# Kernel optimization log

Measured on AMD Instinct MI355X. Metric: run time of the kernel, lower is better.

## Reference

```python
import jax, jax.numpy as jnp
import numpy as np

N = 100000      # nodes
E = 1_000_000   # edges (avg degree ~10)
D_IN = 64
HID = 64
N_CLS = 32


def setup_inputs() -> dict:
    key = jax.random.key(0)
    ks = jax.random.split(key, 9)
    x = jax.random.normal(ks[0], (N, D_IN), dtype=jnp.float32)
    edge_index = jax.random.randint(ks[1], (2, E), 0, N, dtype=jnp.int32)
    s_in = 1.0 / np.sqrt(D_IN)
    s_h = 1.0 / np.sqrt(HID)
    W1 = jax.random.normal(ks[2], (D_IN, HID), dtype=jnp.float32) * s_in
    b1 = jnp.zeros((HID,), dtype=jnp.float32)
    W2 = jax.random.normal(ks[3], (HID, HID), dtype=jnp.float32) * s_h
    b2 = jnp.zeros((HID,), dtype=jnp.float32)
    Wl = jax.random.normal(ks[4], (HID, N_CLS), dtype=jnp.float32) * s_h
    bl = jnp.zeros((N_CLS,), dtype=jnp.float32)
    return {"x": x, "edge_index": edge_index,
            "W1": W1, "b1": b1, "W2": W2, "b2": b2, "Wl": Wl, "bl": bl}


def reference(x, edge_index, W1, b1, W2, b2, Wl, bl):
    # GCNConv default: add self-loops, symmetric normalization D^-1/2 (A+I) D^-1/2
    loop = jnp.arange(N, dtype=edge_index.dtype)
    src = jnp.concatenate([edge_index[0], loop])  # [E+N]
    dst = jnp.concatenate([edge_index[1], loop])  # [E+N]

    deg = jax.ops.segment_sum(jnp.ones_like(dst, dtype=jnp.float32), dst,
                              num_segments=N)              # [N]
    dinv = jnp.where(deg > 0, jax.lax.rsqrt(deg), 0.0)      # D^-1/2
    norm = dinv[src] * dinv[dst]                            # [E+N]

    def gcn_conv(h, W, b):
        h = h @ W                                           # [N, F_out]
        msg = h[src] * norm[:, None]                        # gather + scale
        return jax.ops.segment_sum(msg, dst, num_segments=N) + b

    h = jax.nn.relu(gcn_conv(x, W1, b1))
    h = jax.nn.relu(gcn_conv(h, W2, b2))
    return h @ Wl + bl
```

## Files before the change

### kernel.cpp

```cpp
#include <hip/hip_runtime.h>
#include <hip/hip_fp16.h>
#include <math.h>


#define TPB    256
#define EBLKS  256
#define BSH    9
#define BNODES (1 << BSH)

__global__ __launch_bounds__(TPB)
void k_p1hist(const int* __restrict__ dst, int* __restrict__ OFS,
              int E, int CH, int NBC) {
    __shared__ int h[512];
    int tid = threadIdx.x, b = blockIdx.x;
    for (int i = tid; i < NBC; i += TPB) h[i] = 0;
    __syncthreads();
    int beg = b * CH, end = min(E, beg + CH);
    if (beg < end) {
        int nfull = (end - beg) & ~3;
        for (int i = beg + tid * 4; i < beg + nfull; i += TPB * 4) {
            int4 d = *(const int4*)&dst[i];
            atomicAdd(&h[d.x >> BSH], 1);
            atomicAdd(&h[d.y >> BSH], 1);
            atomicAdd(&h[d.z >> BSH], 1);
            atomicAdd(&h[d.w >> BSH], 1);
        }
        if (tid < (end - beg) - nfull)
            atomicAdd(&h[dst[beg + nfull + tid] >> BSH], 1);
    }
    __syncthreads();
    for (int c = tid; c < NBC; c += TPB) OFS[c * EBLKS + b] = h[c];
}

__global__ __launch_bounds__(TPB)
void k_scanA(const int* __restrict__ OFS, int* __restrict__ bsum, int total) {
    __shared__ int s[TPB];
    int tid = threadIdx.x;
    int i0  = blockIdx.x * 1024 + tid * 4;
    int t = 0;
#pragma unroll
    for (int k = 0; k < 4; ++k) {
        int i = i0 + k;
        t += (i < total) ? OFS[i] : 0;
    }
    s[tid] = t;
    __syncthreads();
    for (int off = TPB / 2; off > 0; off >>= 1) {
        if (tid < off) s[tid] += s[tid + off];
        __syncthreads();
    }
    if (tid == 0) bsum[blockIdx.x] = s[0];
}

__global__ __launch_bounds__(TPB)
void k_scanB(int* bsum, int* OFS, int NBLK, int total, int E) {
    __shared__ int s[TPB];
    int tid = threadIdx.x;
    int v = (tid < NBLK) ? bsum[tid] : 0;
    s[tid] = v;
    __syncthreads();
    for (int off = 1; off < TPB; off <<= 1) {
        int x = (tid >= off) ? s[tid - off] : 0;
        __syncthreads();
        s[tid] += x;
        __syncthreads();
    }
    if (tid < NBLK) bsum[tid] = s[tid] - v;
    if (tid == 0) OFS[total] = E;
}

__global__ __launch_bounds__(TPB)
void k_scanC(int* __restrict__ OFS, const int* __restrict__ bsum, int total) {
    __shared__ int s[TPB];
    int tid = threadIdx.x;
    int i0  = blockIdx.x * 1024 + tid * 4;
    int v[4];
#pragma unroll
    for (int k = 0; k < 4; ++k) {
        int i = i0 + k;
        v[k] = (i < total) ? OFS[i] : 0;
    }
    int tsum = v[0] + v[1] + v[2] + v[3];
    s[tid] = tsum;
    __syncthreads();
    for (int off = 1; off < TPB; off <<= 1) {
        int x = (tid >= off) ? s[tid - off] : 0;
        __syncthreads();
        s[tid] += x;
        __syncthreads();
    }
    int base = bsum[blockIdx.x] + (s[tid] - tsum);
#pragma unroll
    for (int k = 0; k < 4; ++k) {
        int i = i0 + k;
        if (i < total) {
            OFS[i] = base;
            base += v[k];
        }
    }
}

__global__ __launch_bounds__(TPB)
void k_p1scatter(const int* __restrict__ src, const int* __restrict__ dst,
                 const int* __restrict__ OFS, int* __restrict__ ebuf,
                 int E, int CH, int NBC) {
    __shared__ int cur[512];
    int tid = threadIdx.x, b = blockIdx.x;
    for (int c = tid; c < NBC; c += TPB) cur[c] = OFS[c * EBLKS + b];
    __syncthreads();
    int beg = b * CH, end = min(E, beg + CH);
    if (beg >= end) return;
    int nfull = (end - beg) & ~3;
    for (int i = beg + tid * 4; i < beg + nfull; i += TPB * 4) {
        int4 s4 = *(const int4*)&src[i];
        int4 d4 = *(const int4*)&dst[i];
        int p0 = atomicAdd(&cur[d4.x >> BSH], 1);
        int p1 = atomicAdd(&cur[d4.y >> BSH], 1);
        int p2 = atomicAdd(&cur[d4.z >> BSH], 1);
        int p3 = atomicAdd(&cur[d4.w >> BSH], 1);
        ebuf[p0] = (s4.x << BSH) | (d4.x & (BNODES - 1));
        ebuf[p1] = (s4.y << BSH) | (d4.y & (BNODES - 1));
        ebuf[p2] = (s4.z << BSH) | (d4.z & (BNODES - 1));
        ebuf[p3] = (s4.w << BSH) | (d4.w & (BNODES - 1));
    }
    if (tid < (end - beg) - nfull) {
        int i = beg + nfull + tid;
        int d = dst[i];
        int p = atomicAdd(&cur[d >> BSH], 1);
        ebuf[p] = (src[i] << BSH) | (d & (BNODES - 1));
    }
}

__global__ __launch_bounds__(TPB)
void k_p2rowptr(const int* __restrict__ ebuf, const int* __restrict__ OFS,
                int* __restrict__ row_ptr, float* __restrict__ dinv,
                int N, int E, int NBC) {
    __shared__ int cnt[BNODES];
    __shared__ int s1[TPB];
    int tid = threadIdx.x, c = blockIdx.x;
    int beg = OFS[c * EBLKS], end = OFS[(c + 1) * EBLKS];
    for (int i = tid; i < BNODES; i += TPB) cnt[i] = 0;
    __syncthreads();
    for (int i = beg + tid; i < end; i += TPB)
        atomicAdd(&cnt[ebuf[i] & (BNODES - 1)], 1);
    __syncthreads();
    int a0 = cnt[2 * tid], a1 = cnt[2 * tid + 1];
    int pairsum = a0 + a1;
    s1[tid] = pairsum;
    __syncthreads();
    for (int off = 1; off < TPB; off <<= 1) {
        int x = (tid >= off) ? s1[tid - off] : 0;
        __syncthreads();
        s1[tid] += x;
        __syncthreads();
    }
    int ex = s1[tid] - pairsum;
    int node0 = (c << BSH) + 2 * tid;
    if (node0 < N) {
        row_ptr[node0] = beg + ex;
        dinv[node0]    = rsqrtf((float)(a0 + 1));
    }
    if (node0 + 1 < N) {
        row_ptr[node0 + 1] = beg + ex + a0;
        dinv[node0 + 1]    = rsqrtf((float)(a1 + 1));
    }
    if (c == NBC - 1 && tid == 0) row_ptr[N] = E;
}

__global__ __launch_bounds__(TPB)
void k_p2fill(const int* __restrict__ ebuf, const int* __restrict__ OFS,
              const int* __restrict__ row_ptr, const float* __restrict__ dinv,
              int2* __restrict__ colw, int NBC) {
    __shared__ int cnt[BNODES];
    int tid = threadIdx.x, c = blockIdx.x;
    int beg = OFS[c * EBLKS], end = OFS[(c + 1) * EBLKS];
    int cbase = c << BSH;
    for (int i = tid; i < BNODES; i += TPB) cnt[i] = 0;
    __syncthreads();
    for (int i0 = beg + tid; i0 < end; i0 += TPB * 4) {
        int   sv[4], dl[4], pos[4];
        float w[4];
        int   have = 0;
#pragma unroll
        for (int k = 0; k < 4; ++k) {
            int i = i0 + k * TPB;
            if (i < end) {
                int e = ebuf[i];
                sv[k] = e >> BSH;
                dl[k] = e & (BNODES - 1);
                have = k + 1;
            }
        }
#pragma unroll
        for (int k = 0; k < 4; ++k) {
            if (k < have) {
                int r  = atomicAdd(&cnt[dl[k]], 1);
                pos[k] = row_ptr[cbase + dl[k]] + r;
                w[k]   = dinv[sv[k]] * dinv[cbase + dl[k]];
            }
        }
#pragma unroll
        for (int k = 0; k < 4; ++k)
            if (k < have) colw[pos[k]] = make_int2(sv[k], __float_as_int(w[k]));
    }
}

template <int F, bool FINAL, bool HIN, bool HOUT>
__launch_bounds__(256)
__global__ void k_mm(const void* __restrict__ in, const float* __restrict__ W,
                     const float* __restrict__ bias,
                     void* __restrict__ t_out, int n) {
    __shared__ float in_s[64 * 68];
    __shared__ float w_s[64 * F];

    const int tid  = threadIdx.x;
    const int row0 = blockIdx.x * 64;

    for (int i4 = tid; i4 < (64 * F) / 4; i4 += 256)
        ((float4*)w_s)[i4] = ((const float4*)W)[i4];

    if constexpr (HIN) {
        for (int idx = tid; idx < 64 * 8; idx += 256) {
            int r  = idx >> 3;
            int c8 = idx & 7;
            uint4 u = make_uint4(0u, 0u, 0u, 0u);
            if (row0 + r < n)
                u = *(const uint4*)((const __half*)in + (size_t)(row0 + r) * 64 + c8 * 8);
            float2 f0 = __half22float2(*(__half2*)&u.x);
            float2 f1 = __half22float2(*(__half2*)&u.y);
            float2 f2 = __half22float2(*(__half2*)&u.z);
            float2 f3 = __half22float2(*(__half2*)&u.w);
            float* o = &in_s[r * 68 + c8 * 8];
            *(float4*)&o[0] = make_float4(f0.x, f0.y, f1.x, f1.y);
            *(float4*)&o[4] = make_float4(f2.x, f2.y, f3.x, f3.y);
        }
    } else {
        for (int idx = tid; idx < 64 * 16; idx += 256) {
            int r  = idx >> 4;
            int c4 = idx & 15;
            float4 v;
            if (row0 + r < n)
                v = *(const float4*)((const float*)in + (size_t)(row0 + r) * 64 + c4 * 4);
            else
                v = make_float4(0.f, 0.f, 0.f, 0.f);
            *(float4*)&in_s[r * 68 + c4 * 4] = v;
        }
    }
    __syncthreads();

    constexpr int CPT = F / 16;
    const int tx = tid & 15;
    const int ty = tid >> 4;

    float acc[4][CPT];
#pragma unroll
    for (int r = 0; r < 4; ++r)
#pragma unroll
        for (int c = 0; c < CPT; ++c) acc[r][c] = 0.f;

#pragma unroll 4
    for (int k = 0; k < 64; ++k) {
        float b[CPT];
#pragma unroll
        for (int c = 0; c < CPT; ++c) b[c] = w_s[k * F + tx * CPT + c];
#pragma unroll
        for (int r = 0; r < 4; ++r) {
            float a = in_s[(ty * 4 + r) * 68 + k];
#pragma unroll
            for (int c = 0; c < CPT; ++c) acc[r][c] = fmaf(a, b[c], acc[r][c]);
        }
    }

#pragma unroll
    for (int r = 0; r < 4; ++r) {
        int row = row0 + ty * 4 + r;
        if (row >= n) continue;
        if constexpr (HOUT) {
            __half2 p0 = __floats2half2_rn(acc[r][0], acc[r][1]);
            __half2 p1 = __floats2half2_rn(acc[r][2], acc[r][3]);
            uint2 u = make_uint2(*(unsigned*)&p0, *(unsigned*)&p1);
            *(uint2*)((__half*)t_out + (size_t)row * 64 + tx * 4) = u;
        } else {
#pragma unroll
            for (int c = 0; c < CPT; ++c) {
                int col = tx * CPT + c;
                float v = acc[r][c];
                if constexpr (FINAL) v += bias[col];
                ((float*)t_out)[(size_t)row * F + col] = v;
            }
        }
    }
}

__global__ __launch_bounds__(256)
void k_gather(const int* __restrict__ row_ptr, const int2* __restrict__ colw,
              const float* __restrict__ dinv, const float* __restrict__ bias,
              const __half* __restrict__ t, __half* __restrict__ agg, int N) {
    int tid  = threadIdx.x;
    int w    = tid >> 6;
    int lane = tid & 63;
    int g = lane >> 3;
    int p = lane & 7;
    int d = blockIdx.x * 32 + w * 8 + g;

    int beg = 0, end = 0;
    if (d < N) { beg = row_ptr[d]; end = row_ptr[d + 1]; }

    float acc[8];
#pragma unroll
    for (int k = 0; k < 8; ++k) acc[k] = 0.f;

    for (int e = beg; e < end; e += 2) {
        int2 cw0 = colw[e];
        int2 cw1 = (e + 1 < end) ? colw[e + 1] : make_int2(0, 0);
        uint4 a0 = *(const uint4*)(t + (size_t)cw0.x * 64 + p * 8);
        uint4 a1 = *(const uint4*)(t + (size_t)cw1.x * 64 + p * 8);
        float w0 = __int_as_float(cw0.y);
        float w1 = __int_as_float(cw1.y);
        float2 f;
        f = __half22float2(*(__half2*)&a0.x); acc[0] = fmaf(w0, f.x, acc[0]); acc[1] = fmaf(w0, f.y, acc[1]);
        f = __half22float2(*(__half2*)&a0.y); acc[2] = fmaf(w0, f.x, acc[2]); acc[3] = fmaf(w0, f.y, acc[3]);
        f = __half22float2(*(__half2*)&a0.z); acc[4] = fmaf(w0, f.x, acc[4]); acc[5] = fmaf(w0, f.y, acc[5]);
        f = __half22float2(*(__half2*)&a0.w); acc[6] = fmaf(w0, f.x, acc[6]); acc[7] = fmaf(w0, f.y, acc[7]);
        f = __half22float2(*(__half2*)&a1.x); acc[0] = fmaf(w1, f.x, acc[0]); acc[1] = fmaf(w1, f.y, acc[1]);
        f = __half22float2(*(__half2*)&a1.y); acc[2] = fmaf(w1, f.x, acc[2]); acc[3] = fmaf(w1, f.y, acc[3]);
        f = __half22float2(*(__half2*)&a1.z); acc[4] = fmaf(w1, f.x, acc[4]); acc[5] = fmaf(w1, f.y, acc[5]);
        f = __half22float2(*(__half2*)&a1.w); acc[6] = fmaf(w1, f.x, acc[6]); acc[7] = fmaf(w1, f.y, acc[7]);
    }

    if (d < N) {
        float dd = dinv[d];
        float w2 = dd * dd;
        uint4 a = *(const uint4*)(t + (size_t)d * 64 + p * 8);
        float4 b0 = *(const float4*)&bias[p * 8];
        float4 b1 = *(const float4*)&bias[p * 8 + 4];
        float2 s0 = __half22float2(*(__half2*)&a.x);
        float2 s1 = __half22float2(*(__half2*)&a.y);
        float2 s2 = __half22float2(*(__half2*)&a.z);
        float2 s3 = __half22float2(*(__half2*)&a.w);
        float o0 = fmaxf(fmaf(w2, s0.x, acc[0]) + b0.x, 0.f);
        float o1 = fmaxf(fmaf(w2, s0.y, acc[1]) + b0.y, 0.f);
        float o2 = fmaxf(fmaf(w2, s1.x, acc[2]) + b0.z, 0.f);
        float o3 = fmaxf(fmaf(w2, s1.y, acc[3]) + b0.w, 0.f);
        float o4 = fmaxf(fmaf(w2, s2.x, acc[4]) + b1.x, 0.f);
        float o5 = fmaxf(fmaf(w2, s2.y, acc[5]) + b1.y, 0.f);
        float o6 = fmaxf(fmaf(w2, s3.x, acc[6]) + b1.z, 0.f);
        float o7 = fmaxf(fmaf(w2, s3.y, acc[7]) + b1.w, 0.f);
        __half2 h0 = __floats2half2_rn(o0, o1);
        __half2 h1 = __floats2half2_rn(o2, o3);
        __half2 h2 = __floats2half2_rn(o4, o5);
        __half2 h3 = __floats2half2_rn(o6, o7);
        uint4 u = make_uint4(*(unsigned*)&h0, *(unsigned*)&h1,
                             *(unsigned*)&h2, *(unsigned*)&h3);
        *(uint4*)(agg + (size_t)d * 64 + p * 8) = u;
    }
}

extern "C" void kernel_launch(void* const* d_in, const int* in_sizes, int n_in,
                              void* d_out, int out_size, void* d_ws, size_t ws_size,
                              hipStream_t stream) {
    const float* x  = (const float*)d_in[0];
    const int*   ei = (const int*)d_in[1];
    const float* W1 = (const float*)d_in[2];
    const float* b1 = (const float*)d_in[3];
    const float* W2 = (const float*)d_in[4];
    const float* b2 = (const float*)d_in[5];
    const float* Wl = (const float*)d_in[6];
    const float* bl = (const float*)d_in[7];
    float*       out = (float*)d_out;

    const int N = in_sizes[0] / 64;
    const int E = in_sizes[1] / 2;
    const int* srcp = ei;
    const int* dstp = ei + E;

    const int NBC   = (N + BNODES - 1) / BNODES;
    const int CH    = (((E + EBLKS - 1) / EBLKS) + 3) & ~3;
    const int total = NBC * EBLKS;
    const int NBLK  = (total + 1023) / 1024;

    char*  ws  = (char*)d_ws;
    size_t off = 0;
    auto alloc = [&](size_t bytes) -> void* {
        void* p = (void*)(ws + off);
        off += (bytes + 255) & ~(size_t)255;
        return p;
    };
    int*    OFS     = (int*)alloc(((size_t)total + 1) * 4);
    int*    bsum    = (int*)alloc((size_t)NBLK * 4);
    int*    ebuf    = (int*)alloc((size_t)E * 4);
    int*    row_ptr = (int*)alloc((size_t)(N + 1) * 4);
    float*  dinv    = (float*)alloc((size_t)N * 4);
    int2*   colw    = (int2*)alloc((size_t)E * 8);
    __half* t       = (__half*)alloc((size_t)N * 64 * 2);
    __half* agg1    = (__half*)alloc((size_t)N * 64 * 2);
    __half* agg2    = agg1;

    const int nb_mm = (N + 63) / 64;
    const int nb_g  = (N + 31) / 32;

    k_p1hist   <<<EBLKS, TPB, 0, stream>>>(dstp, OFS, E, CH, NBC);
    k_scanA    <<<NBLK,  TPB, 0, stream>>>(OFS, bsum, total);
    k_scanB    <<<1,     TPB, 0, stream>>>(bsum, OFS, NBLK, total, E);
    k_scanC    <<<NBLK,  TPB, 0, stream>>>(OFS, bsum, total);
    k_p1scatter<<<EBLKS, TPB, 0, stream>>>(srcp, dstp, OFS, ebuf, E, CH, NBC);
    k_p2rowptr <<<NBC,   TPB, 0, stream>>>(ebuf, OFS, row_ptr, dinv, N, E, NBC);
    k_p2fill   <<<NBC,   TPB, 0, stream>>>(ebuf, OFS, row_ptr, dinv, colw, NBC);

    k_mm<64, false, false, true><<<nb_mm, 256, 0, stream>>>(x, W1, nullptr, t, N);
    k_gather<<<nb_g, 256, 0, stream>>>(row_ptr, colw, dinv, b1, t, agg1, N);

    k_mm<64, false, true, true><<<nb_mm, 256, 0, stream>>>(agg1, W2, nullptr, t, N);
    k_gather<<<nb_g, 256, 0, stream>>>(row_ptr, colw, dinv, b2, t, agg2, N);

    k_mm<32, true, true, false><<<nb_mm, 256, 0, stream>>>(agg2, Wl, bl, out, N);
}
```

Measured before the change: 217.4 us.

## Fuse gather-aggregation into following matmul and merge scan kernels

Each gather/aggregation stage now runs inside the following dense matmul kernel: the aggregated rows go straight into shared memory, so the fp16 intermediate agg buffer is no longer written and read back. The single-block scanB kernel is removed, and each scanC block computes its own prefix of block sums with a wave reduction. The last-bucket end offset now comes from E instead of OFS[total]. The aim is fewer launches and less global traffic, at the cost of the gather now running on 64-row blocks with fewer total waves, which may reduce latency hiding.

```diff
diff --git a/kernel.cpp b/kernel.cpp
--- a/kernel.cpp
+++ b/kernel.cpp
@@ -53,11 +53,26 @@
 }
 
 __global__ __launch_bounds__(TPB)
-void k_scanB(int* bsum, int* OFS, int NBLK, int total, int E) {
+void k_scanC(int* __restrict__ OFS, const int* __restrict__ bsum,
+             int NBLK, int total) {
     __shared__ int s[TPB];
+    __shared__ int pfx;
     int tid = threadIdx.x;
-    int v = (tid < NBLK) ? bsum[tid] : 0;
-    s[tid] = v;
+    if (tid < 64) {
+        int v = (tid < NBLK && tid < (int)blockIdx.x) ? bsum[tid] : 0;
+#pragma unroll
+        for (int off = 1; off < 64; off <<= 1) v += __shfl_xor(v, off);
+        if (tid == 0) pfx = v;
+    }
+    int i0 = blockIdx.x * 1024 + tid * 4;
+    int v[4];
+#pragma unroll
+    for (int k = 0; k < 4; ++k) {
+        int i = i0 + k;
+        v[k] = (i < total) ? OFS[i] : 0;
+    }
+    int tsum = v[0] + v[1] + v[2] + v[3];
+    s[tid] = tsum;
     __syncthreads();
     for (int off = 1; off < TPB; off <<= 1) {
         int x = (tid >= off) ? s[tid - off] : 0;
@@ -65,31 +80,7 @@
         s[tid] += x;
         __syncthreads();
     }
-    if (tid < NBLK) bsum[tid] = s[tid] - v;
-    if (tid == 0) OFS[total] = E;
-}
-
-__global__ __launch_bounds__(TPB)
-void k_scanC(int* __restrict__ OFS, const int* __restrict__ bsum, int total) {
-    __shared__ int s[TPB];
-    int tid = threadIdx.x;
-    int i0  = blockIdx.x * 1024 + tid * 4;
-    int v[4];
-#pragma unroll
-    for (int k = 0; k < 4; ++k) {
-        int i = i0 + k;
-        v[k] = (i < total) ? OFS[i] : 0;
-    }
-    int tsum = v[0] + v[1] + v[2] + v[3];
-    s[tid] = tsum;
-    __syncthreads();
-    for (int off = 1; off < TPB; off <<= 1) {
-        int x = (tid >= off) ? s[tid - off] : 0;
-        __syncthreads();
-        s[tid] += x;
-        __syncthreads();
-    }
-    int base = bsum[blockIdx.x] + (s[tid] - tsum);
+    int base = pfx + (s[tid] - tsum);
 #pragma unroll
     for (int k = 0; k < 4; ++k) {
         int i = i0 + k;
@@ -138,7 +129,8 @@
     __shared__ int cnt[BNODES];
     __shared__ int s1[TPB];
     int tid = threadIdx.x, c = blockIdx.x;
-    int beg = OFS[c * EBLKS], end = OFS[(c + 1) * EBLKS];
+    int beg = OFS[c * EBLKS];
+    int end = (c == NBC - 1) ? E : OFS[(c + 1) * EBLKS];
     for (int i = tid; i < BNODES; i += TPB) cnt[i] = 0;
     __syncthreads();
     for (int i = beg + tid; i < end; i += TPB)
@@ -170,10 +162,11 @@
 __global__ __launch_bounds__(TPB)
 void k_p2fill(const int* __restrict__ ebuf, const int* __restrict__ OFS,
               const int* __restrict__ row_ptr, const float* __restrict__ dinv,
-              int2* __restrict__ colw, int NBC) {
+              int2* __restrict__ colw, int E, int NBC) {
     __shared__ int cnt[BNODES];
     int tid = threadIdx.x, c = blockIdx.x;
-    int beg = OFS[c * EBLKS], end = OFS[(c + 1) * EBLKS];
+    int beg = OFS[c * EBLKS];
+    int end = (c == NBC - 1) ? E : OFS[(c + 1) * EBLKS];
     int cbase = c << BSH;
     for (int i = tid; i < BNODES; i += TPB) cnt[i] = 0;
     __syncthreads();
@@ -205,11 +198,69 @@
     }
 }
 
-template <int F, bool FINAL, bool HIN, bool HOUT>
 __launch_bounds__(256)
-__global__ void k_mm(const void* __restrict__ in, const float* __restrict__ W,
-                     const float* __restrict__ bias,
-                     void* __restrict__ t_out, int n) {
+__global__ void k_mm1(const float* __restrict__ in, const float* __restrict__ W,
+                      __half* __restrict__ t_out, int n) {
+    __shared__ float in_s[64 * 68];
+    __shared__ float w_s[64 * 64];
+
+    const int tid  = threadIdx.x;
+    const int row0 = blockIdx.x * 64;
+
+    for (int i4 = tid; i4 < (64 * 64) / 4; i4 += 256)
+        ((float4*)w_s)[i4] = ((const float4*)W)[i4];
+
+    for (int idx = tid; idx < 64 * 16; idx += 256) {
+        int r  = idx >> 4;
+        int c4 = idx & 15;
+        float4 v;
+        if (row0 + r < n)
+            v = *(const float4*)&in[(size_t)(row0 + r) * 64 + c4 * 4];
+        else
+            v = make_float4(0.f, 0.f, 0.f, 0.f);
+        *(float4*)&in_s[r * 68 + c4 * 4] = v;
+    }
+    __syncthreads();
+
+    const int tx = tid & 15;
+    const int ty = tid >> 4;
+
+    float acc[4][4];
+#pragma unroll
+    for (int r = 0; r < 4; ++r)
+#pragma unroll
+        for (int c = 0; c < 4; ++c) acc[r][c] = 0.f;
+
+#pragma unroll 4
+    for (int k = 0; k < 64; ++k) {
+        float b[4];
+#pragma unroll
+        for (int c = 0; c < 4; ++c) b[c] = w_s[k * 64 + tx * 4 + c];
+#pragma unroll
+        for (int r = 0; r < 4; ++r) {
+            float a = in_s[(ty * 4 + r) * 68 + k];
+#pragma unroll
+            for (int c = 0; c < 4; ++c) acc[r][c] = fmaf(a, b[c], acc[r][c]);
+        }
+    }
+
+#pragma unroll
+    for (int r = 0; r < 4; ++r) {
+        int row = row0 + ty * 4 + r;
+        if (row >= n) continue;
+        __half2 p0 = __floats2half2_rn(acc[r][0], acc[r][1]);
+        __half2 p1 = __floats2half2_rn(acc[r][2], acc[r][3]);
+        uint2 u = make_uint2(*(unsigned*)&p0, *(unsigned*)&p1);
+        *(uint2*)(t_out + (size_t)row * 64 + tx * 4) = u;
+    }
+}
+
+template <int F, bool FINAL>
+__launch_bounds__(256)
+__global__ void k_gmm(const int* __restrict__ row_ptr, const int2* __restrict__ colw,
+                      const float* __restrict__ dinv, const float* __restrict__ gbias,
+                      const __half* __restrict__ t, const float* __restrict__ W,
+                      const float* __restrict__ fbias, void* __restrict__ out, int n) {
     __shared__ float in_s[64 * 68];
     __shared__ float w_s[64 * F];
 
@@ -219,32 +270,62 @@
     for (int i4 = tid; i4 < (64 * F) / 4; i4 += 256)
         ((float4*)w_s)[i4] = ((const float4*)W)[i4];
 
-    if constexpr (HIN) {
-        for (int idx = tid; idx < 64 * 8; idx += 256) {
-            int r  = idx >> 3;
-            int c8 = idx & 7;
-            uint4 u = make_uint4(0u, 0u, 0u, 0u);
-            if (row0 + r < n)
-                u = *(const uint4*)((const __half*)in + (size_t)(row0 + r) * 64 + c8 * 8);
-            float2 f0 = __half22float2(*(__half2*)&u.x);
-            float2 f1 = __half22float2(*(__half2*)&u.y);
-            float2 f2 = __half22float2(*(__half2*)&u.z);
-            float2 f3 = __half22float2(*(__half2*)&u.w);
-            float* o = &in_s[r * 68 + c8 * 8];
-            *(float4*)&o[0] = make_float4(f0.x, f0.y, f1.x, f1.y);
-            *(float4*)&o[4] = make_float4(f2.x, f2.y, f3.x, f3.y);
-        }
-    } else {
-        for (int idx = tid; idx < 64 * 16; idx += 256) {
-            int r  = idx >> 4;
-            int c4 = idx & 15;
-            float4 v;
-            if (row0 + r < n)
-                v = *(const float4*)((const float*)in + (size_t)(row0 + r) * 64 + c4 * 4);
-            else
-                v = make_float4(0.f, 0.f, 0.f, 0.f);
-            *(float4*)&in_s[r * 68 + c4 * 4] = v;
-        }
+    const int wv   = tid >> 6;
+    const int lane = tid & 63;
+    const int g    = lane >> 3;
+    const int p    = lane & 7;
+    float4 gb0 = *(const float4*)&gbias[p * 8];
+    float4 gb1 = *(const float4*)&gbias[p * 8 + 4];
+
+#pragma unroll
+    for (int round = 0; round < 2; ++round) {
+        int m = round * 32 + wv * 8 + g;
+        int d = row0 + m;
+        float acc[8];
+#pragma unroll
+        for (int k = 0; k < 8; ++k) acc[k] = 0.f;
+        float o[8];
+        if (d < n) {
+            int beg = row_ptr[d], end = row_ptr[d + 1];
+            for (int e = beg; e < end; e += 2) {
+                int2 cw0 = colw[e];
+                int2 cw1 = (e + 1 < end) ? colw[e + 1] : make_int2(0, 0);
+                uint4 a0 = *(const uint4*)(t + (size_t)cw0.x * 64 + p * 8);
+                uint4 a1 = *(const uint4*)(t + (size_t)cw1.x * 64 + p * 8);
+                float w0 = __int_as_float(cw0.y);
+                float w1 = __int_as_float(cw1.y);
+                float2 f;
+                f = __half22float2(*(__half2*)&a0.x); acc[0] = fmaf(w0, f.x, acc[0]); acc[1] = fmaf(w0, f.y, acc[1]);
+                f = __half22float2(*(__half2*)&a0.y); acc[2] = fmaf(w0, f.x, acc[2]); acc[3] = fmaf(w0, f.y, acc[3]);
+                f = __half22float2(*(__half2*)&a0.z); acc[4] = fmaf(w0, f.x, acc[4]); acc[5] = fmaf(w0, f.y, acc[5]);
+                f = __half22float2(*(__half2*)&a0.w); acc[6] = fmaf(w0, f.x, acc[6]); acc[7] = fmaf(w0, f.y, acc[7]);
+                f = __half22float2(*(__half2*)&a1.x); acc[0] = fmaf(w1, f.x, acc[0]); acc[1] = fmaf(w1, f.y, acc[1]);
+                f = __half22float2(*(__half2*)&a1.y); acc[2] = fmaf(w1, f.x, acc[2]); acc[3] = fmaf(w1, f.y, acc[3]);
+                f = __half22float2(*(__half2*)&a1.z); acc[4] = fmaf(w1, f.x, acc[4]); acc[5] = fmaf(w1, f.y, acc[5]);
+                f = __half22float2(*(__half2*)&a1.w); acc[6] = fmaf(w1, f.x, acc[6]); acc[7] = fmaf(w1, f.y, acc[7]);
+            }
+            float dd = dinv[d];
+            float w2 = dd * dd;
+            uint4 a = *(const uint4*)(t + (size_t)d * 64 + p * 8);
+            float2 s0 = __half22float2(*(__half2*)&a.x);
+            float2 s1 = __half22float2(*(__half2*)&a.y);
+            float2 s2 = __half22float2(*(__half2*)&a.z);
+            float2 s3 = __half22float2(*(__half2*)&a.w);
+            o[0] = fmaxf(fmaf(w2, s0.x, acc[0]) + gb0.x, 0.f);
+            o[1] = fmaxf(fmaf(w2, s0.y, acc[1]) + gb0.y, 0.f);
+            o[2] = fmaxf(fmaf(w2, s1.x, acc[2]) + gb0.z, 0.f);
+            o[3] = fmaxf(fmaf(w2, s1.y, acc[3]) + gb0.w, 0.f);
+            o[4] = fmaxf(fmaf(w2, s2.x, acc[4]) + gb1.x, 0.f);
+            o[5] = fmaxf(fmaf(w2, s2.y, acc[5]) + gb1.y, 0.f);
+            o[6] = fmaxf(fmaf(w2, s3.x, acc[6]) + gb1.z, 0.f);
+            o[7] = fmaxf(fmaf(w2, s3.y, acc[7]) + gb1.w, 0.f);
+        } else {
+#pragma unroll
+            for (int k = 0; k < 8; ++k) o[k] = 0.f;
+        }
+        float* ls = &in_s[m * 68 + p * 8];
+        *(float4*)&ls[0] = make_float4(o[0], o[1], o[2], o[3]);
+        *(float4*)&ls[4] = make_float4(o[4], o[5], o[6], o[7]);
     }
     __syncthreads();
 
@@ -275,84 +356,18 @@
     for (int r = 0; r < 4; ++r) {
         int row = row0 + ty * 4 + r;
         if (row >= n) continue;
-        if constexpr (HOUT) {
+        if constexpr (FINAL) {
+#pragma unroll
+            for (int c = 0; c < CPT; ++c) {
+                int col = tx * CPT + c;
+                ((float*)out)[(size_t)row * F + col] = acc[r][c] + fbias[col];
+            }
+        } else {
             __half2 p0 = __floats2half2_rn(acc[r][0], acc[r][1]);
             __half2 p1 = __floats2half2_rn(acc[r][2], acc[r][3]);
             uint2 u = make_uint2(*(unsigned*)&p0, *(unsigned*)&p1);
-            *(uint2*)((__half*)t_out + (size_t)row * 64 + tx * 4) = u;
-        } else {
-#pragma unroll
-            for (int c = 0; c < CPT; ++c) {
-                int col = tx * CPT + c;
-                float v = acc[r][c];
-                if constexpr (FINAL) v += bias[col];
-                ((float*)t_out)[(size_t)row * F + col] = v;
-            }
-        }
-    }
-}
-
-__global__ __launch_bounds__(256)
-void k_gather(const int* __restrict__ row_ptr, const int2* __restrict__ colw,
-              const float* __restrict__ dinv, const float* __restrict__ bias,
-              const __half* __restrict__ t, __half* __restrict__ agg, int N) {
-    int tid  = threadIdx.x;
-    int w    = tid >> 6;
-    int lane = tid & 63;
-    int g = lane >> 3;
-    int p = lane & 7;
-    int d = blockIdx.x * 32 + w * 8 + g;
-
-    int beg = 0, end = 0;
-    if (d < N) { beg = row_ptr[d]; end = row_ptr[d + 1]; }
-
-    float acc[8];
-#pragma unroll
-    for (int k = 0; k < 8; ++k) acc[k] = 0.f;
-
-    for (int e = beg; e < end; e += 2) {
-        int2 cw0 = colw[e];
-        int2 cw1 = (e + 1 < end) ? colw[e + 1] : make_int2(0, 0);
-        uint4 a0 = *(const uint4*)(t + (size_t)cw0.x * 64 + p * 8);
-        uint4 a1 = *(const uint4*)(t + (size_t)cw1.x * 64 + p * 8);
-        float w0 = __int_as_float(cw0.y);
-        float w1 = __int_as_float(cw1.y);
-        float2 f;
-        f = __half22float2(*(__half2*)&a0.x); acc[0] = fmaf(w0, f.x, acc[0]); acc[1] = fmaf(w0, f.y, acc[1]);
-        f = __half22float2(*(__half2*)&a0.y); acc[2] = fmaf(w0, f.x, acc[2]); acc[3] = fmaf(w0, f.y, acc[3]);
-        f = __half22float2(*(__half2*)&a0.z); acc[4] = fmaf(w0, f.x, acc[4]); acc[5] = fmaf(w0, f.y, acc[5]);
-        f = __half22float2(*(__half2*)&a0.w); acc[6] = fmaf(w0, f.x, acc[6]); acc[7] = fmaf(w0, f.y, acc[7]);
-        f = __half22float2(*(__half2*)&a1.x); acc[0] = fmaf(w1, f.x, acc[0]); acc[1] = fmaf(w1, f.y, acc[1]);
-        f = __half22float2(*(__half2*)&a1.y); acc[2] = fmaf(w1, f.x, acc[2]); acc[3] = fmaf(w1, f.y, acc[3]);
-        f = __half22float2(*(__half2*)&a1.z); acc[4] = fmaf(w1, f.x, acc[4]); acc[5] = fmaf(w1, f.y, acc[5]);
-        f = __half22float2(*(__half2*)&a1.w); acc[6] = fmaf(w1, f.x, acc[6]); acc[7] = fmaf(w1, f.y, acc[7]);
-    }
-
-    if (d < N) {
-        float dd = dinv[d];
-        float w2 = dd * dd;
-        uint4 a = *(const uint4*)(t + (size_t)d * 64 + p * 8);
-        float4 b0 = *(const float4*)&bias[p * 8];
-        float4 b1 = *(const float4*)&bias[p * 8 + 4];
-        float2 s0 = __half22float2(*(__half2*)&a.x);
-        float2 s1 = __half22float2(*(__half2*)&a.y);
-        float2 s2 = __half22float2(*(__half2*)&a.z);
-        float2 s3 = __half22float2(*(__half2*)&a.w);
-        float o0 = fmaxf(fmaf(w2, s0.x, acc[0]) + b0.x, 0.f);
-        float o1 = fmaxf(fmaf(w2, s0.y, acc[1]) + b0.y, 0.f);
-        float o2 = fmaxf(fmaf(w2, s1.x, acc[2]) + b0.z, 0.f);
-        float o3 = fmaxf(fmaf(w2, s1.y, acc[3]) + b0.w, 0.f);
-        float o4 = fmaxf(fmaf(w2, s2.x, acc[4]) + b1.x, 0.f);
-        float o5 = fmaxf(fmaf(w2, s2.y, acc[5]) + b1.y, 0.f);
-        float o6 = fmaxf(fmaf(w2, s3.x, acc[6]) + b1.z, 0.f);
-        float o7 = fmaxf(fmaf(w2, s3.y, acc[7]) + b1.w, 0.f);
-        __half2 h0 = __floats2half2_rn(o0, o1);
-        __half2 h1 = __floats2half2_rn(o2, o3);
-        __half2 h2 = __floats2half2_rn(o4, o5);
-        __half2 h3 = __floats2half2_rn(o6, o7);
-        uint4 u = make_uint4(*(unsigned*)&h0, *(unsigned*)&h1,
-                             *(unsigned*)&h2, *(unsigned*)&h3);
-        *(uint4*)(agg + (size_t)d * 64 + p * 8) = u;
+            *(uint2*)((__half*)out + (size_t)row * 64 + tx * 4) = u;
+        }
     }
 }
 
@@ -392,26 +407,23 @@
     int*    row_ptr = (int*)alloc((size_t)(N + 1) * 4);
     float*  dinv    = (float*)alloc((size_t)N * 4);
     int2*   colw    = (int2*)alloc((size_t)E * 8);
-    __half* t       = (__half*)alloc((size_t)N * 64 * 2);
-    __half* agg1    = (__half*)alloc((size_t)N * 64 * 2);
-    __half* agg2    = agg1;
+    __half* t1      = (__half*)alloc((size_t)N * 64 * 2);
+    __half* t2      = (__half*)alloc((size_t)N * 64 * 2);
 
     const int nb_mm = (N + 63) / 64;
-    const int nb_g  = (N + 31) / 32;
 
     k_p1hist   <<<EBLKS, TPB, 0, stream>>>(dstp, OFS, E, CH, NBC);
     k_scanA    <<<NBLK,  TPB, 0, stream>>>(OFS, bsum, total);
-    k_scanB    <<<1,     TPB, 0, stream>>>(bsum, OFS, NBLK, total, E);
-    k_scanC    <<<NBLK,  TPB, 0, stream>>>(OFS, bsum, total);
+    k_scanC    <<<NBLK,  TPB, 0, stream>>>(OFS, bsum, NBLK, total);
     k_p1scatter<<<EBLKS, TPB, 0, stream>>>(srcp, dstp, OFS, ebuf, E, CH, NBC);
     k_p2rowptr <<<NBC,   TPB, 0, stream>>>(ebuf, OFS, row_ptr, dinv, N, E, NBC);
-    k_p2fill   <<<NBC,   TPB, 0, stream>>>(ebuf, OFS, row_ptr, dinv, colw, NBC);
-
-    k_mm<64, false, false, true><<<nb_mm, 256, 0, stream>>>(x, W1, nullptr, t, N);
-    k_gather<<<nb_g, 256, 0, stream>>>(row_ptr, colw, dinv, b1, t, agg1, N);
-
-    k_mm<64, false, true, true><<<nb_mm, 256, 0, stream>>>(agg1, W2, nullptr, t, N);
-    k_gather<<<nb_g, 256, 0, stream>>>(row_ptr, colw, dinv, b2, t, agg2, N);
-
-    k_mm<32, true, true, false><<<nb_mm, 256, 0, stream>>>(agg2, Wl, bl, out, N);
-}
+    k_p2fill   <<<NBC,   TPB, 0, stream>>>(ebuf, OFS, row_ptr, dinv, colw, E, NBC);
+
+    k_mm1<<<nb_mm, 256, 0, stream>>>(x, W1, t1, N);
+
+    k_gmm<64, false><<<nb_mm, 256, 0, stream>>>(row_ptr, colw, dinv, b1, t1,
+                                                W2, nullptr, t2, N);
+
+    k_gmm<32, true><<<nb_mm, 256, 0, stream>>>(row_ptr, colw, dinv, b2, t2,
+                                               Wl, bl, out, N);
+}
```

Result: no change. 220.2 us (+1.3%).

## Factor GCN normalization into matmul rows, drop edge weights, merge CSR kernels

Applied to the files above, without the earlier changes.

Each matmul now pre-scales its output rows by dinv[src], and the gather multiplies the summed neighbour features by dinv[dst] once per node. This lets the edge list store only source indices (4 bytes instead of 8), which cuts edge-stream traffic and the per-edge multiply. The row-pointer and fill kernels are fused into one kernel that keeps per-node offsets in shared memory, and the single-block scan stage is folded into the final scan via a wave-level prefix of the block sums. A zero padding row at index N handles odd-length neighbour lists. The cost is that fp16 rounding now happens on pre-scaled values.

```diff
diff --git a/kernel.cpp b/kernel.cpp
--- a/kernel.cpp
+++ b/kernel.cpp
@@ -53,11 +53,26 @@
 }
 
 __global__ __launch_bounds__(TPB)
-void k_scanB(int* bsum, int* OFS, int NBLK, int total, int E) {
+void k_scanC(int* __restrict__ OFS, const int* __restrict__ bsum,
+             int NBLK, int total) {
     __shared__ int s[TPB];
+    __shared__ int pfx;
     int tid = threadIdx.x;
-    int v = (tid < NBLK) ? bsum[tid] : 0;
-    s[tid] = v;
+    if (tid < 64) {
+        int v = (tid < NBLK && tid < (int)blockIdx.x) ? bsum[tid] : 0;
+#pragma unroll
+        for (int off = 1; off < 64; off <<= 1) v += __shfl_xor(v, off);
+        if (tid == 0) pfx = v;
+    }
+    int i0 = blockIdx.x * 1024 + tid * 4;
+    int v[4];
+#pragma unroll
+    for (int k = 0; k < 4; ++k) {
+        int i = i0 + k;
+        v[k] = (i < total) ? OFS[i] : 0;
+    }
+    int tsum = v[0] + v[1] + v[2] + v[3];
+    s[tid] = tsum;
     __syncthreads();
     for (int off = 1; off < TPB; off <<= 1) {
         int x = (tid >= off) ? s[tid - off] : 0;
@@ -65,31 +80,7 @@
         s[tid] += x;
         __syncthreads();
     }
-    if (tid < NBLK) bsum[tid] = s[tid] - v;
-    if (tid == 0) OFS[total] = E;
-}
-
-__global__ __launch_bounds__(TPB)
-void k_scanC(int* __restrict__ OFS, const int* __restrict__ bsum, int total) {
-    __shared__ int s[TPB];
-    int tid = threadIdx.x;
-    int i0  = blockIdx.x * 1024 + tid * 4;
-    int v[4];
-#pragma unroll
-    for (int k = 0; k < 4; ++k) {
-        int i = i0 + k;
-        v[k] = (i < total) ? OFS[i] : 0;
-    }
-    int tsum = v[0] + v[1] + v[2] + v[3];
-    s[tid] = tsum;
-    __syncthreads();
-    for (int off = 1; off < TPB; off <<= 1) {
-        int x = (tid >= off) ? s[tid - off] : 0;
-        __syncthreads();
-        s[tid] += x;
-        __syncthreads();
-    }
-    int base = bsum[blockIdx.x] + (s[tid] - tsum);
+    int base = pfx + (s[tid] - tsum);
 #pragma unroll
     for (int k = 0; k < 4; ++k) {
         int i = i0 + k;
@@ -132,13 +123,15 @@
 }
 
 __global__ __launch_bounds__(TPB)
-void k_p2rowptr(const int* __restrict__ ebuf, const int* __restrict__ OFS,
-                int* __restrict__ row_ptr, float* __restrict__ dinv,
-                int N, int E, int NBC) {
+void k_p2(const int* __restrict__ ebuf, const int* __restrict__ OFS,
+          int* __restrict__ row_ptr, float* __restrict__ dinv,
+          int* __restrict__ colw, int N, int E, int NBC) {
     __shared__ int cnt[BNODES];
+    __shared__ int ofs[BNODES];
     __shared__ int s1[TPB];
     int tid = threadIdx.x, c = blockIdx.x;
-    int beg = OFS[c * EBLKS], end = OFS[(c + 1) * EBLKS];
+    int beg = OFS[c * EBLKS];
+    int end = (c == NBC - 1) ? E : OFS[(c + 1) * EBLKS];
     for (int i = tid; i < BNODES; i += TPB) cnt[i] = 0;
     __syncthreads();
     for (int i = beg + tid; i < end; i += TPB)
@@ -156,6 +149,8 @@
     }
     int ex = s1[tid] - pairsum;
     int node0 = (c << BSH) + 2 * tid;
+    ofs[2 * tid]     = beg + ex;
+    ofs[2 * tid + 1] = beg + ex + a0;
     if (node0 < N) {
         row_ptr[node0] = beg + ex;
         dinv[node0]    = rsqrtf((float)(a0 + 1));
@@ -165,22 +160,12 @@
         dinv[node0 + 1]    = rsqrtf((float)(a1 + 1));
     }
     if (c == NBC - 1 && tid == 0) row_ptr[N] = E;
-}
-
-__global__ __launch_bounds__(TPB)
-void k_p2fill(const int* __restrict__ ebuf, const int* __restrict__ OFS,
-              const int* __restrict__ row_ptr, const float* __restrict__ dinv,
-              int2* __restrict__ colw, int NBC) {
-    __shared__ int cnt[BNODES];
-    int tid = threadIdx.x, c = blockIdx.x;
-    int beg = OFS[c * EBLKS], end = OFS[(c + 1) * EBLKS];
-    int cbase = c << BSH;
-    for (int i = tid; i < BNODES; i += TPB) cnt[i] = 0;
+    cnt[2 * tid] = 0;
+    cnt[2 * tid + 1] = 0;
     __syncthreads();
     for (int i0 = beg + tid; i0 < end; i0 += TPB * 4) {
-        int   sv[4], dl[4], pos[4];
-        float w[4];
-        int   have = 0;
+        int sv[4], dl[4], pos[4];
+        int have = 0;
 #pragma unroll
         for (int k = 0; k < 4; ++k) {
             int i = i0 + k * TPB;
@@ -195,21 +180,20 @@
         for (int k = 0; k < 4; ++k) {
             if (k < have) {
                 int r  = atomicAdd(&cnt[dl[k]], 1);
-                pos[k] = row_ptr[cbase + dl[k]] + r;
-                w[k]   = dinv[sv[k]] * dinv[cbase + dl[k]];
+                pos[k] = ofs[dl[k]] + r;
             }
         }
 #pragma unroll
         for (int k = 0; k < 4; ++k)
-            if (k < have) colw[pos[k]] = make_int2(sv[k], __float_as_int(w[k]));
-    }
-}
-
-template <int F, bool FINAL, bool HIN, bool HOUT>
+            if (k < have) colw[pos[k]] = sv[k];
+    }
+}
+
+template <int F, bool FINAL, bool HIN>
 __launch_bounds__(256)
 __global__ void k_mm(const void* __restrict__ in, const float* __restrict__ W,
-                     const float* __restrict__ bias,
-                     void* __restrict__ t_out, int n) {
+                     const float* __restrict__ bias, const float* __restrict__ dinv,
+                     void* __restrict__ out, int n) {
     __shared__ float in_s[64 * 68];
     __shared__ float w_s[64 * F];
 
@@ -275,33 +259,36 @@
     for (int r = 0; r < 4; ++r) {
         int row = row0 + ty * 4 + r;
         if (row >= n) continue;
-        if constexpr (HOUT) {
-            __half2 p0 = __floats2half2_rn(acc[r][0], acc[r][1]);
-            __half2 p1 = __floats2half2_rn(acc[r][2], acc[r][3]);
-            uint2 u = make_uint2(*(unsigned*)&p0, *(unsigned*)&p1);
-            *(uint2*)((__half*)t_out + (size_t)row * 64 + tx * 4) = u;
-        } else {
+        if constexpr (FINAL) {
 #pragma unroll
             for (int c = 0; c < CPT; ++c) {
                 int col = tx * CPT + c;
-                float v = acc[r][c];
-                if constexpr (FINAL) v += bias[col];
-                ((float*)t_out)[(size_t)row * F + col] = v;
+                ((float*)out)[(size_t)row * F + col] = acc[r][c] + bias[col];
             }
-        }
+        } else {
+            float dd = dinv[row];
+            __half2 p0 = __floats2half2_rn(acc[r][0] * dd, acc[r][1] * dd);
+            __half2 p1 = __floats2half2_rn(acc[r][2] * dd, acc[r][3] * dd);
+            uint2 u = make_uint2(*(unsigned*)&p0, *(unsigned*)&p1);
+            *(uint2*)((__half*)out + (size_t)row * 64 + tx * 4) = u;
+        }
+    }
+    if constexpr (!FINAL) {
+        if (blockIdx.x == 0 && tid < 16)
+            *(uint2*)((__half*)out + (size_t)n * 64 + tid * 4) = make_uint2(0u, 0u);
     }
 }
 
 __global__ __launch_bounds__(256)
-void k_gather(const int* __restrict__ row_ptr, const int2* __restrict__ colw,
+void k_gather(const int* __restrict__ row_ptr, const int* __restrict__ colw,
               const float* __restrict__ dinv, const float* __restrict__ bias,
               const __half* __restrict__ t, __half* __restrict__ agg, int N) {
     int tid  = threadIdx.x;
-    int w    = tid >> 6;
+    int wv   = tid >> 6;
     int lane = tid & 63;
     int g = lane >> 3;
     int p = lane & 7;
-    int d = blockIdx.x * 32 + w * 8 + g;
+    int d = blockIdx.x * 32 + wv * 8 + g;
 
     int beg = 0, end = 0;
     if (d < N) { beg = row_ptr[d]; end = row_ptr[d + 1]; }
@@ -311,26 +298,23 @@
     for (int k = 0; k < 8; ++k) acc[k] = 0.f;
 
     for (int e = beg; e < end; e += 2) {
-        int2 cw0 = colw[e];
-        int2 cw1 = (e + 1 < end) ? colw[e + 1] : make_int2(0, 0);
-        uint4 a0 = *(const uint4*)(t + (size_t)cw0.x * 64 + p * 8);
-        uint4 a1 = *(const uint4*)(t + (size_t)cw1.x * 64 + p * 8);
-        float w0 = __int_as_float(cw0.y);
-        float w1 = __int_as_float(cw1.y);
+        int s0 = colw[e];
+        int s1 = (e + 1 < end) ? colw[e + 1] : N;
+        uint4 a0 = *(const uint4*)(t + (size_t)s0 * 64 + p * 8);
+        uint4 a1 = *(const uint4*)(t + (size_t)s1 * 64 + p * 8);
         float2 f;
-        f = __half22float2(*(__half2*)&a0.x); acc[0] = fmaf(w0, f.x, acc[0]); acc[1] = fmaf(w0, f.y, acc[1]);
-        f = __half22float2(*(__half2*)&a0.y); acc[2] = fmaf(w0, f.x, acc[2]); acc[3] = fmaf(w0, f.y, acc[3]);
-        f = __half22float2(*(__half2*)&a0.z); acc[4] = fmaf(w0, f.x, acc[4]); acc[5] = fmaf(w0, f.y, acc[5]);
-        f = __half22float2(*(__half2*)&a0.w); acc[6] = fmaf(w0, f.x, acc[6]); acc[7] = fmaf(w0, f.y, acc[7]);
-        f = __half22float2(*(__half2*)&a1.x); acc[0] = fmaf(w1, f.x, acc[0]); acc[1] = fmaf(w1, f.y, acc[1]);
-        f = __half22float2(*(__half2*)&a1.y); acc[2] = fmaf(w1, f.x, acc[2]); acc[3] = fmaf(w1, f.y, acc[3]);
-        f = __half22float2(*(__half2*)&a1.z); acc[4] = fmaf(w1, f.x, acc[4]); acc[5] = fmaf(w1, f.y, acc[5]);
-        f = __half22float2(*(__half2*)&a1.w); acc[6] = fmaf(w1, f.x, acc[6]); acc[7] = fmaf(w1, f.y, acc[7]);
+        f = __half22float2(*(__half2*)&a0.x); acc[0] += f.x; acc[1] += f.y;
+        f = __half22float2(*(__half2*)&a0.y); acc[2] += f.x; acc[3] += f.y;
+        f = __half22float2(*(__half2*)&a0.z); acc[4] += f.x; acc[5] += f.y;
+        f = __half22float2(*(__half2*)&a0.w); acc[6] += f.x; acc[7] += f.y;
+        f = __half22float2(*(__half2*)&a1.x); acc[0] += f.x; acc[1] += f.y;
+        f = __half22float2(*(__half2*)&a1.y); acc[2] += f.x; acc[3] += f.y;
+        f = __half22float2(*(__half2*)&a1.z); acc[4] += f.x; acc[5] += f.y;
+        f = __half22float2(*(__half2*)&a1.w); acc[6] += f.x; acc[7] += f.y;
     }
 
     if (d < N) {
         float dd = dinv[d];
-        float w2 = dd * dd;
         uint4 a = *(const uint4*)(t + (size_t)d * 64 + p * 8);
         float4 b0 = *(const float4*)&bias[p * 8];
         float4 b1 = *(const float4*)&bias[p * 8 + 4];
@@ -338,14 +322,14 @@
         float2 s1 = __half22float2(*(__half2*)&a.y);
         float2 s2 = __half22float2(*(__half2*)&a.z);
         float2 s3 = __half22float2(*(__half2*)&a.w);
-        float o0 = fmaxf(fmaf(w2, s0.x, acc[0]) + b0.x, 0.f);
-        float o1 = fmaxf(fmaf(w2, s0.y, acc[1]) + b0.y, 0.f);
-        float o2 = fmaxf(fmaf(w2, s1.x, acc[2]) + b0.z, 0.f);
-        float o3 = fmaxf(fmaf(w2, s1.y, acc[3]) + b0.w, 0.f);
-        float o4 = fmaxf(fmaf(w2, s2.x, acc[4]) + b1.x, 0.f);
-        float o5 = fmaxf(fmaf(w2, s2.y, acc[5]) + b1.y, 0.f);
-        float o6 = fmaxf(fmaf(w2, s3.x, acc[6]) + b1.z, 0.f);
-        float o7 = fmaxf(fmaf(w2, s3.y, acc[7]) + b1.w, 0.f);
+        float o0 = fmaxf(fmaf(dd, acc[0] + s0.x, b0.x), 0.f);
+        float o1 = fmaxf(fmaf(dd, acc[1] + s0.y, b0.y), 0.f);
+        float o2 = fmaxf(fmaf(dd, acc[2] + s1.x, b0.z), 0.f);
+        float o3 = fmaxf(fmaf(dd, acc[3] + s1.y, b0.w), 0.f);
+        float o4 = fmaxf(fmaf(dd, acc[4] + s2.x, b1.x), 0.f);
+        float o5 = fmaxf(fmaf(dd, acc[5] + s2.y, b1.y), 0.f);
+        float o6 = fmaxf(fmaf(dd, acc[6] + s3.x, b1.z), 0.f);
+        float o7 = fmaxf(fmaf(dd, acc[7] + s3.y, b1.w), 0.f);
         __half2 h0 = __floats2half2_rn(o0, o1);
         __half2 h1 = __floats2half2_rn(o2, o3);
         __half2 h2 = __floats2half2_rn(o4, o5);
@@ -391,9 +375,10 @@
     int*    ebuf    = (int*)alloc((size_t)E * 4);
     int*    row_ptr = (int*)alloc((size_t)(N + 1) * 4);
     float*  dinv    = (float*)alloc((size_t)N * 4);
-    int2*   colw    = (int2*)alloc((size_t)E * 8);
-    __half* t       = (__half*)alloc((size_t)N * 64 * 2);
+    int*    colw    = (int*)alloc((size_t)E * 4);
+    __half* t1      = (__half*)alloc((size_t)(N + 1) * 64 * 2);
     __half* agg1    = (__half*)alloc((size_t)N * 64 * 2);
+    __half* t2      = t1;
     __half* agg2    = agg1;
 
     const int nb_mm = (N + 63) / 64;
@@ -401,17 +386,15 @@
 
     k_p1hist   <<<EBLKS, TPB, 0, stream>>>(dstp, OFS, E, CH, NBC);
     k_scanA    <<<NBLK,  TPB, 0, stream>>>(OFS, bsum, total);
-    k_scanB    <<<1,     TPB, 0, stream>>>(bsum, OFS, NBLK, total, E);
-    k_scanC    <<<NBLK,  TPB, 0, stream>>>(OFS, bsum, total);
+    k_scanC    <<<NBLK,  TPB, 0, stream>>>(OFS, bsum, NBLK, total);
     k_p1scatter<<<EBLKS, TPB, 0, stream>>>(srcp, dstp, OFS, ebuf, E, CH, NBC);
-    k_p2rowptr <<<NBC,   TPB, 0, stream>>>(ebuf, OFS, row_ptr, dinv, N, E, NBC);
-    k_p2fill   <<<NBC,   TPB, 0, stream>>>(ebuf, OFS, row_ptr, dinv, colw, NBC);
-
-    k_mm<64, false, false, true><<<nb_mm, 256, 0, stream>>>(x, W1, nullptr, t, N);
-    k_gather<<<nb_g, 256, 0, stream>>>(row_ptr, colw, dinv, b1, t, agg1, N);
-
-    k_mm<64, false, true, true><<<nb_mm, 256, 0, stream>>>(agg1, W2, nullptr, t, N);
-    k_gather<<<nb_g, 256, 0, stream>>>(row_ptr, colw, dinv, b2, t, agg2, N);
-
-    k_mm<32, true, true, false><<<nb_mm, 256, 0, stream>>>(agg2, Wl, bl, out, N);
-}
+    k_p2       <<<NBC,   TPB, 0, stream>>>(ebuf, OFS, row_ptr, dinv, colw, N, E, NBC);
+
+    k_mm<64, false, false><<<nb_mm, 256, 0, stream>>>(x, W1, nullptr, dinv, t1, N);
+    k_gather<<<nb_g, 256, 0, stream>>>(row_ptr, colw, dinv, b1, t1, agg1, N);
+
+    k_mm<64, false, true><<<nb_mm, 256, 0, stream>>>(agg1, W2, nullptr, dinv, t2, N);
+    k_gather<<<nb_g, 256, 0, stream>>>(row_ptr, colw, dinv, b2, t2, agg2, N);
+
+    k_mm<32, true, true><<<nb_mm, 256, 0, stream>>>(agg2, Wl, bl, nullptr, out, N);
+}
```

New measurement: 209.7 us. 1.04x faster.
